# Kernel optimization log

Measured on AMD Instinct MI355X. Metric: run time of the kernel, lower is better.

## Reference

```python
import jax, jax.numpy as jnp
import numpy as np

NUM_HEADS = 16
D_IN = 1024
D_OUT = 64  # = D_IN // NUM_HEADS
N = 2048


def setup_inputs() -> dict:
    key = jax.random.key(0)
    kx, kq, kk, kv, ko = jax.random.split(key, 5)
    x = jax.random.normal(kx, (N, D_IN), dtype=jnp.float32)
    # per-head projection weights, stacked over heads (torch code keeps a
    # Python list of SelfAttention modules; stacking is the vectorized form)
    q_proj = jax.random.normal(kq, (NUM_HEADS, D_IN, D_OUT), dtype=jnp.float32)
    k_proj = jax.random.normal(kk, (NUM_HEADS, D_IN, D_OUT), dtype=jnp.float32)
    v_proj = jax.random.normal(kv, (NUM_HEADS, D_IN, D_OUT), dtype=jnp.float32)
    o_proj = jax.random.normal(ko, (D_IN, D_IN), dtype=jnp.float32)
    return {"x": x, "q_proj": q_proj, "k_proj": k_proj, "v_proj": v_proj, "o_proj": o_proj}


def reference(x, q_proj, k_proj, v_proj, o_proj):
    d_out = q_proj.shape[-1]
    # per-head projections: [H, N, E]
    q = jnp.einsum('nd,hde->hne', x, q_proj)
    k = jnp.einsum('nd,hde->hne', x, k_proj)
    v = jnp.einsum('nd,hde->hne', x, v_proj)
    # full NxN scores per head (matches the naive torch implementation's math)
    scores = jnp.einsum('hne,hme->hnm', q, k) / jnp.sqrt(jnp.float32(d_out))
    attn = jax.nn.softmax(scores, axis=-1)
    ctx = jnp.einsum('hnm,hme->hne', attn, v)
    # concat heads along the feature dim (head 0 first, as in torch.cat)
    h, n, e = ctx.shape
    out = jnp.transpose(ctx, (1, 0, 2)).reshape(n, h * e)
    return out @ o_proj
```

## Files before the change

kernel.cpp:

```cpp
#include <hip/hip_runtime.h>

#define H 16
#define N 2048
#define E 64
#define D 1024

typedef __attribute__((ext_vector_type(8))) short bf16x8;
typedef __attribute__((ext_vector_type(4))) float f32x4;

__device__ __forceinline__ float bf2f(unsigned short u) {
    union { unsigned int i; float f; } v;
    v.i = ((unsigned int)u) << 16;
    return v.f;
}
__device__ __forceinline__ unsigned short f2bf(float f) {
    unsigned int u = __float_as_uint(f);
    return (unsigned short)((u + 0x7fffu + ((u >> 16) & 1u)) >> 16);
}
#define MFMA(a, b, c) __builtin_amdgcn_mfma_f32_16x16x32_bf16(a, b, c, 0, 0, 0)

typedef __attribute__((address_space(3))) unsigned int lds_u32;
typedef const __attribute__((address_space(1))) unsigned int glb_u32;
__device__ __forceinline__ void dma16(const unsigned short* g, unsigned short* l) {
    __builtin_amdgcn_global_load_lds((glb_u32*)g, (lds_u32*)l, 16, 0, 0);
}

__device__ __forceinline__ int sw8(int row, int c)  { return row * 64  + ((c ^ (row & 7)) << 3); }
__device__ __forceinline__ int sw16(int row, int c) { return row * 128 + ((c ^ (row & 7)) << 3); }

__global__ __launch_bounds__(256) void convert_all_kernel(
    const float* __restrict__ x,
    const float* __restrict__ qw, const float* __restrict__ kw,
    const float* __restrict__ vw, const float* __restrict__ ow,
    unsigned short* __restrict__ xh, unsigned short* __restrict__ xl,
    unsigned short* __restrict__ wBh, unsigned short* __restrict__ wBl,
    unsigned short* __restrict__ wvt, unsigned short* __restrict__ woh)
{
    __shared__ float ts[64][65];
    const int b0 = blockIdx.x;
    const int t = threadIdx.x;
    if (b0 < 2048) {
        const int i = (b0 * 256 + t) * 4;
        const float4 v = *(const float4*)&x[i];
        ushort4 hh, ll;
        hh.x = f2bf(v.x); ll.x = f2bf(v.x - bf2f(hh.x));
        hh.y = f2bf(v.y); ll.y = f2bf(v.y - bf2f(hh.y));
        hh.z = f2bf(v.z); ll.z = f2bf(v.z - bf2f(hh.z));
        hh.w = f2bf(v.w); ll.w = f2bf(v.w - bf2f(hh.w));
        *(ushort4*)&xh[i] = hh;
        *(ushort4*)&xl[i] = ll;
        return;
    }
    const int b = b0 - 2048;
    const float* src;
    int rs, dt, orow0;
    bool has_lo;
    unsigned short *dh, *dl;
    if (b < 768) {
        const int which = b >> 8, r = b & 255, h = r >> 4;
        dt = r & 15;
        src = (which == 0 ? qw : which == 1 ? kw : vw) + ((size_t)h * D + dt * 64) * E;
        rs = E;
        if (which == 0)      { dh = wBh; dl = wBl; orow0 = h * 64;        has_lo = true; }
        else if (which == 1) { dh = wBh; dl = wBl; orow0 = 1024 + h * 64; has_lo = true; }
        else                 { dh = wvt; dl = wBl; orow0 = h * 64;        has_lo = false; }
    } else {
        const int r = b - 768, ct = r >> 4;
        dt = r & 15;
        src = ow + (size_t)(dt * 64) * D + ct * 64;
        rs = D;
        orow0 = ct * 64;
        dh = woh; dl = wBl; has_lo = false;
    }
    {
        const int row = t >> 2, cb = (t & 3) * 16;
        #pragma unroll
        for (int j = 0; j < 16; j += 4) {
            const float4 v = *(const float4*)&src[row * rs + cb + j];
            ts[row][cb + j + 0] = v.x;
            ts[row][cb + j + 1] = v.y;
            ts[row][cb + j + 2] = v.z;
            ts[row][cb + j + 3] = v.w;
        }
    }
    __syncthreads();
    {
        const int cl = t >> 2, dp = (t & 3) * 16;
        bf16x8 hv0, hv1, lv0, lv1;
        #pragma unroll
        for (int i = 0; i < 16; ++i) {
            const float f = ts[dp + i][cl];
            const unsigned short hh = f2bf(f);
            const unsigned short lo = f2bf(f - bf2f(hh));
            if (i < 8) { hv0[i] = (short)hh; lv0[i] = (short)lo; }
            else       { hv1[i - 8] = (short)hh; lv1[i - 8] = (short)lo; }
        }
        const size_t o = (size_t)(orow0 + cl) * D + dt * 64 + dp;
        *(bf16x8*)&dh[o] = hv0;
        *(bf16x8*)&dh[o + 8] = hv1;
        if (has_lo) {
            *(bf16x8*)&dl[o] = lv0;
            *(bf16x8*)&dl[o + 8] = lv1;
        }
    }
}

__global__ __launch_bounds__(256, 3) void qkv_kernel(
    const unsigned short* __restrict__ xh, const unsigned short* __restrict__ xl,
    const unsigned short* __restrict__ wBh, const unsigned short* __restrict__ wBl,
    const unsigned short* __restrict__ wvt,
    unsigned short* __restrict__ Qh, unsigned short* __restrict__ Ql,
    unsigned short* __restrict__ Kh, unsigned short* __restrict__ Kl,
    unsigned short* __restrict__ Vt)
{
    __shared__ unsigned short ash[128 * 64], asl[128 * 64];
    __shared__ unsigned short bsh[64 * 64], bsl[64 * 64];
    const int n0 = blockIdx.x * 128;
    const int ct0 = blockIdx.y;
    const int sec = ct0 >> 4;
    const int hh = ct0 & 15;
    const bool isv = (sec == 2);
    const unsigned short* Bh = isv ? wvt : wBh;
    const size_t brow0 = (sec == 1 ? 1024 : 0) + hh * 64;

    const int t = threadIdx.x;
    const int lane = t & 63, wvi = t >> 6, quad = lane >> 4, l15 = lane & 15;

    f32x4 acc[2][4];
    #pragma unroll
    for (int i = 0; i < 2; ++i)
        #pragma unroll
        for (int j = 0; j < 4; ++j) acc[i][j] = (f32x4){0.f, 0.f, 0.f, 0.f};

    for (int k0 = 0; k0 < D; k0 += 64) {
        __syncthreads();
        #pragma unroll
        for (int p = 0; p < 4; ++p) {
            const int row = p * 32 + wvi * 8 + (lane >> 3);
            const int lc = (lane & 7) ^ (row & 7);
            const int lo = p * 2048 + wvi * 512 + lane * 8;
            const size_t ga = (size_t)(n0 + row) * D + k0 + lc * 8;
            dma16(&xh[ga], &ash[lo]);
            if (!isv) dma16(&xl[ga], &asl[lo]);
        }
        #pragma unroll
        for (int p = 0; p < 2; ++p) {
            const int row = p * 32 + wvi * 8 + (lane >> 3);
            const int lc = (lane & 7) ^ (row & 7);
            const int lo = p * 2048 + wvi * 512 + lane * 8;
            const size_t gb = (brow0 + row) * D + k0 + lc * 8;
            dma16(&Bh[gb], &bsh[lo]);
            if (!isv) dma16(&wBl[gb], &bsl[lo]);
        }
        __syncthreads();

        #pragma unroll
        for (int kwi = 0; kwi < 2; ++kwi) {
            const int c = kwi * 4 + quad;
            bf16x8 ah[2], al[2], bh[4], bl[4];
            #pragma unroll
            for (int i = 0; i < 2; ++i) {
                ah[i] = *(const bf16x8*)&ash[sw8(wvi * 32 + i * 16 + l15, c)];
                if (!isv) al[i] = *(const bf16x8*)&asl[sw8(wvi * 32 + i * 16 + l15, c)];
            }
            #pragma unroll
            for (int j = 0; j < 4; ++j) {
                bh[j] = *(const bf16x8*)&bsh[sw8(j * 16 + l15, c)];
                if (!isv) bl[j] = *(const bf16x8*)&bsl[sw8(j * 16 + l15, c)];
            }
            #pragma unroll
            for (int i = 0; i < 2; ++i)
                #pragma unroll
                for (int j = 0; j < 4; ++j) {
                    acc[i][j] = MFMA(ah[i], bh[j], acc[i][j]);
                    if (!isv) {
                        acc[i][j] = MFMA(ah[i], bl[j], acc[i][j]);
                        acc[i][j] = MFMA(al[i], bh[j], acc[i][j]);
                    }
                }
        }
    }

    if (isv) {
        #pragma unroll
        for (int j = 0; j < 4; ++j) {
            const int e = j * 16 + l15;
            #pragma unroll
            for (int i = 0; i < 2; ++i) {
                const int nb = n0 + wvi * 32 + i * 16 + quad * 4;
                ushort4 pk;
                pk.x = f2bf(acc[i][j][0]);
                pk.y = f2bf(acc[i][j][1]);
                pk.z = f2bf(acc[i][j][2]);
                pk.w = f2bf(acc[i][j][3]);
                *(ushort4*)&Vt[((size_t)hh * 64 + e) * N + nb] = pk;
            }
        }
    } else {
        const float scale = (sec == 0) ? 0.125f : 1.0f;
        unsigned short* Oh = (sec == 0) ? Qh : Kh;
        unsigned short* Ol = (sec == 0) ? Ql : Kl;
        #pragma unroll
        for (int j = 0; j < 4; ++j) {
            const int e = j * 16 + l15;
            #pragma unroll
            for (int i = 0; i < 2; ++i)
                #pragma unroll
                for (int r = 0; r < 4; ++r) {
                    const int n = n0 + wvi * 32 + i * 16 + quad * 4 + r;
                    const float val = acc[i][j][r] * scale;
                    const unsigned short hv = f2bf(val);
                    Oh[((size_t)hh * N + n) * E + e] = hv;
                    Ol[((size_t)hh * N + n) * E + e] = f2bf(val - bf2f(hv));
                }
        }
    }
}

__global__ __launch_bounds__(256, 2) void attn_kernel(
    const unsigned short* __restrict__ Qh, const unsigned short* __restrict__ Ql,
    const unsigned short* __restrict__ Kh, const unsigned short* __restrict__ Kl,
    const unsigned short* __restrict__ Vt,
    unsigned short* __restrict__ Ch)
{
    __shared__ unsigned short ksh[128 * 64], ksl[128 * 64];
    __shared__ unsigned short vts[64 * 128];
    __shared__ unsigned short ps[4 * 16 * 136];
    const int r0 = blockIdx.x * 64, h = blockIdx.y;
    const int t = threadIdx.x, lane = t & 63, wvi = t >> 6, quad = lane >> 4, l15 = lane & 15;

    bf16x8 qfh[2], qfl[2];
    {
        const size_t base = ((size_t)h * N + r0 + wvi * 16 + l15) * E;
        #pragma unroll
        for (int kwi = 0; kwi < 2; ++kwi) {
            qfh[kwi] = *(const bf16x8*)&Qh[base + kwi * 32 + quad * 8];
            qfl[kwi] = *(const bf16x8*)&Ql[base + kwi * 32 + quad * 8];
        }
    }

    f32x4 oacc[4];
    #pragma unroll
    for (int ct = 0; ct < 4; ++ct) oacc[ct] = (f32x4){0.f, 0.f, 0.f, 0.f};
    float mrow[4] = {-1e30f, -1e30f, -1e30f, -1e30f};
    float lrow[4] = {0.f, 0.f, 0.f, 0.f};

    for (int m0 = 0; m0 < N; m0 += 128) {
        __syncthreads();
        #pragma unroll
        for (int p = 0; p < 4; ++p) {
            const int row = p * 32 + wvi * 8 + (lane >> 3);
            const int lc = (lane & 7) ^ (row & 7);
            const int lo = p * 2048 + wvi * 512 + lane * 8;
            const size_t gk = ((size_t)h * N + m0 + row) * E + lc * 8;
            dma16(&Kh[gk], &ksh[lo]);
            dma16(&Kl[gk], &ksl[lo]);
        }
        #pragma unroll
        for (int p = 0; p < 4; ++p) {
            const int row = p * 16 + wvi * 4 + (lane >> 4);
            const int lc = (lane & 15) ^ (row & 7);
            const int lo = p * 2048 + wvi * 512 + lane * 8;
            dma16(&Vt[((size_t)h * 64 + row) * N + m0 + lc * 8], &vts[lo]);
        }
        __syncthreads();

        f32x4 s[8];
        #pragma unroll
        for (int ct = 0; ct < 8; ++ct) s[ct] = (f32x4){0.f, 0.f, 0.f, 0.f};
        #pragma unroll
        for (int kwi = 0; kwi < 2; ++kwi) {
            const int c = kwi * 4 + quad;
            #pragma unroll
            for (int ct = 0; ct < 8; ++ct) {
                const bf16x8 bh = *(const bf16x8*)&ksh[sw8(ct * 16 + l15, c)];
                const bf16x8 bl = *(const bf16x8*)&ksl[sw8(ct * 16 + l15, c)];
                s[ct] = MFMA(qfh[kwi], bh, s[ct]);
                s[ct] = MFMA(qfh[kwi], bl, s[ct]);
                s[ct] = MFMA(qfl[kwi], bh, s[ct]);
            }
        }

        #pragma unroll
        for (int r = 0; r < 4; ++r) {
            float mx = s[0][r];
            #pragma unroll
            for (int ct = 1; ct < 8; ++ct) mx = fmaxf(mx, s[ct][r]);
            mx = fmaxf(mx, __shfl_xor(mx, 1));
            mx = fmaxf(mx, __shfl_xor(mx, 2));
            mx = fmaxf(mx, __shfl_xor(mx, 4));
            mx = fmaxf(mx, __shfl_xor(mx, 8));
            const float mn = fmaxf(mrow[r], mx);
            const float alpha = __expf(mrow[r] - mn);
            mrow[r] = mn;
            float sum = 0.f;
            #pragma unroll
            for (int ct = 0; ct < 8; ++ct) {
                const float p = __expf(s[ct][r] - mn);
                s[ct][r] = p;
                sum += p;
            }
            sum += __shfl_xor(sum, 1);
            sum += __shfl_xor(sum, 2);
            sum += __shfl_xor(sum, 4);
            sum += __shfl_xor(sum, 8);
            lrow[r] = lrow[r] * alpha + sum;
            #pragma unroll
            for (int ct = 0; ct < 4; ++ct) oacc[ct][r] *= alpha;
        }

        #pragma unroll
        for (int ct = 0; ct < 8; ++ct)
            #pragma unroll
            for (int r = 0; r < 4; ++r)
                ps[(wvi * 16 + quad * 4 + r) * 136 + ct * 16 + l15] = f2bf(s[ct][r]);

        #pragma unroll
        for (int kwi = 0; kwi < 4; ++kwi) {
            const bf16x8 pa = *(const bf16x8*)&ps[(wvi * 16 + l15) * 136 + kwi * 32 + quad * 8];
            #pragma unroll
            for (int ct = 0; ct < 4; ++ct) {
                const bf16x8 vb = *(const bf16x8*)&vts[sw16(ct * 16 + l15, kwi * 4 + quad)];
                oacc[ct] = MFMA(pa, vb, oacc[ct]);
            }
        }
    }

    #pragma unroll
    for (int r = 0; r < 4; ++r) {
        const float inv = 1.f / lrow[r];
        const int n = r0 + wvi * 16 + quad * 4 + r;
        #pragma unroll
        for (int ct = 0; ct < 4; ++ct)
            Ch[(size_t)n * D + h * 64 + ct * 16 + l15] = f2bf(oacc[ct][r] * inv);
    }
}

__global__ __launch_bounds__(256, 4) void out_proj_kernel(
    const unsigned short* __restrict__ Chh, const unsigned short* __restrict__ Wh,
    float* __restrict__ out)
{
    __shared__ unsigned short ash[64 * 64], bsh[64 * 64];
    const int n0 = blockIdx.x * 64, c0 = blockIdx.y * 64;
    const int t = threadIdx.x, lane = t & 63, wvi = t >> 6, quad = lane >> 4, l15 = lane & 15;

    f32x4 acc[4];
    #pragma unroll
    for (int j = 0; j < 4; ++j) acc[j] = (f32x4){0.f, 0.f, 0.f, 0.f};

    for (int k0 = 0; k0 < D; k0 += 64) {
        __syncthreads();
        #pragma unroll
        for (int p = 0; p < 2; ++p) {
            const int row = p * 32 + wvi * 8 + (lane >> 3);
            const int lc = (lane & 7) ^ (row & 7);
            const int lo = p * 2048 + wvi * 512 + lane * 8;
            dma16(&Chh[(size_t)(n0 + row) * D + k0 + lc * 8], &ash[lo]);
            dma16(&Wh[(size_t)(c0 + row) * D + k0 + lc * 8], &bsh[lo]);
        }
        __syncthreads();

        #pragma unroll
        for (int kwi = 0; kwi < 2; ++kwi) {
            const int c = kwi * 4 + quad;
            const bf16x8 ah = *(const bf16x8*)&ash[sw8(wvi * 16 + l15, c)];
            #pragma unroll
            for (int j = 0; j < 4; ++j) {
                const bf16x8 bh = *(const bf16x8*)&bsh[sw8(j * 16 + l15, c)];
                acc[j] = MFMA(ah, bh, acc[j]);
            }
        }
    }

    #pragma unroll
    for (int r = 0; r < 4; ++r) {
        const int n = n0 + wvi * 16 + quad * 4 + r;
        #pragma unroll
        for (int j = 0; j < 4; ++j)
            out[(size_t)n * D + c0 + j * 16 + l15] = acc[j][r];
    }
}

extern "C" void kernel_launch(void* const* d_in, const int* in_sizes, int n_in,
                              void* d_out, int out_size, void* d_ws, size_t ws_size,
                              hipStream_t stream) {
    const float* x  = (const float*)d_in[0];
    const float* qw = (const float*)d_in[1];
    const float* kw = (const float*)d_in[2];
    const float* vw = (const float*)d_in[3];
    const float* ow = (const float*)d_in[4];
    float* out = (float*)d_out;

    unsigned short* ws = (unsigned short*)d_ws;
    const size_t M1 = 1024 * 1024;
    unsigned short* wBh = ws;
    unsigned short* wBl = ws + 2 * M1;
    unsigned short* wvt = ws + 4 * M1;
    unsigned short* woh = ws + 5 * M1;
    unsigned short* xh  = ws + 6 * M1;
    unsigned short* xl  = ws + 8 * M1;
    unsigned short* Qh  = ws + 10 * M1;
    unsigned short* Ql  = ws + 12 * M1;
    unsigned short* Kh  = ws + 14 * M1;
    unsigned short* Kl  = ws + 16 * M1;
    unsigned short* Vt  = ws + 18 * M1;
    unsigned short* Ch  = xh;

    convert_all_kernel<<<3072, 256, 0, stream>>>(x, qw, kw, vw, ow,
                                                 xh, xl, wBh, wBl, wvt, woh);
    qkv_kernel<<<dim3(16, 48), 256, 0, stream>>>(xh, xl, wBh, wBl, wvt,
                                                 Qh, Ql, Kh, Kl, Vt);
    attn_kernel<<<dim3(32, 16), 256, 0, stream>>>(Qh, Ql, Kh, Kl, Vt, Ch);
    out_proj_kernel<<<dim3(32, 16), 256, 0, stream>>>(Ch, woh, out);
}
```

Before: 181.1 us.

## Double-buffer K/V tiles in attention with fp16 PV and exp2 softmax

Restructures the attention loop to use 64-key tiles with a two-stage LDS double buffer, so the DMA for the next K/V tile is issued before computing the current one and one barrier per iteration is removed. V and P switch from bf16 to fp16 (packed RTZ conversion) for the PV MFMA, which gives more mantissa precision. The log2(e) factor is folded into the Q scale so softmax can use exp2f. Smaller tiles cut LDS use and register pressure but double the loop trip count, and overlap correctness depends on the barrier placement before each buffer is reused.

```diff
diff --git a/kernel.cpp b/kernel.cpp
--- a/kernel.cpp
+++ b/kernel.cpp
@@ -6,6 +6,8 @@
 #define D 1024
 
 typedef __attribute__((ext_vector_type(8))) short bf16x8;
+typedef __attribute__((ext_vector_type(8))) _Float16 f16x8;
+typedef __attribute__((ext_vector_type(2))) __fp16 fp16v2;
 typedef __attribute__((ext_vector_type(4))) float f32x4;
 
 __device__ __forceinline__ float bf2f(unsigned short u) {
@@ -17,7 +19,8 @@
     unsigned int u = __float_as_uint(f);
     return (unsigned short)((u + 0x7fffu + ((u >> 16) & 1u)) >> 16);
 }
-#define MFMA(a, b, c) __builtin_amdgcn_mfma_f32_16x16x32_bf16(a, b, c, 0, 0, 0)
+#define MFMA(a, b, c)  __builtin_amdgcn_mfma_f32_16x16x32_bf16(a, b, c, 0, 0, 0)
+#define MFMAH(a, b, c) __builtin_amdgcn_mfma_f32_16x16x32_f16(a, b, c, 0, 0, 0)
 
 typedef __attribute__((address_space(3))) unsigned int lds_u32;
 typedef const __attribute__((address_space(1))) unsigned int glb_u32;
@@ -26,7 +29,6 @@
 }
 
 __device__ __forceinline__ int sw8(int row, int c)  { return row * 64  + ((c ^ (row & 7)) << 3); }
-__device__ __forceinline__ int sw16(int row, int c) { return row * 128 + ((c ^ (row & 7)) << 3); }
 
 __global__ __launch_bounds__(256) void convert_all_kernel(
     const float* __restrict__ x,
@@ -188,16 +190,15 @@
             #pragma unroll
             for (int i = 0; i < 2; ++i) {
                 const int nb = n0 + wvi * 32 + i * 16 + quad * 4;
-                ushort4 pk;
-                pk.x = f2bf(acc[i][j][0]);
-                pk.y = f2bf(acc[i][j][1]);
-                pk.z = f2bf(acc[i][j][2]);
-                pk.w = f2bf(acc[i][j][3]);
-                *(ushort4*)&Vt[((size_t)hh * 64 + e) * N + nb] = pk;
+                union { fp16v2 h; unsigned int u; } c01, c23;
+                c01.h = __builtin_amdgcn_cvt_pkrtz(acc[i][j][0], acc[i][j][1]);
+                c23.h = __builtin_amdgcn_cvt_pkrtz(acc[i][j][2], acc[i][j][3]);
+                uint2 pk = {c01.u, c23.u};
+                *(uint2*)&Vt[((size_t)hh * 64 + e) * N + nb] = pk;
             }
         }
     } else {
-        const float scale = (sec == 0) ? 0.125f : 1.0f;
+        const float scale = (sec == 0) ? 0.125f * 1.44269504f : 1.0f;
         unsigned short* Oh = (sec == 0) ? Qh : Kh;
         unsigned short* Ol = (sec == 0) ? Ql : Kl;
         #pragma unroll
@@ -223,11 +224,13 @@
     const unsigned short* __restrict__ Vt,
     unsigned short* __restrict__ Ch)
 {
-    __shared__ unsigned short ksh[128 * 64], ksl[128 * 64];
-    __shared__ unsigned short vts[64 * 128];
-    __shared__ unsigned short ps[4 * 16 * 136];
+    __shared__ unsigned short kb[2][3][64 * 64];
+    __shared__ unsigned short ps[4 * 16 * 72];
     const int r0 = blockIdx.x * 64, h = blockIdx.y;
     const int t = threadIdx.x, lane = t & 63, wvi = t >> 6, quad = lane >> 4, l15 = lane & 15;
+
+    const int srow0 = wvi * 8 + (lane >> 3);
+    const int slo0  = wvi * 512 + lane * 8;
 
     bf16x8 qfh[2], qfl[2];
     {
@@ -245,36 +248,44 @@
     float mrow[4] = {-1e30f, -1e30f, -1e30f, -1e30f};
     float lrow[4] = {0.f, 0.f, 0.f, 0.f};
 
-    for (int m0 = 0; m0 < N; m0 += 128) {
+    #pragma unroll
+    for (int p = 0; p < 2; ++p) {
+        const int row = p * 32 + srow0;
+        const int lc = (lane & 7) ^ (row & 7);
+        const int lo = p * 2048 + slo0;
+        const size_t gk = ((size_t)h * N + row) * E + lc * 8;
+        dma16(&Kh[gk], &kb[0][0][lo]);
+        dma16(&Kl[gk], &kb[0][1][lo]);
+        dma16(&Vt[((size_t)h * 64 + row) * N + lc * 8], &kb[0][2][lo]);
+    }
+
+    for (int mt = 0; mt < N / 64; ++mt) {
+        const int b = mt & 1;
         __syncthreads();
-        #pragma unroll
-        for (int p = 0; p < 4; ++p) {
-            const int row = p * 32 + wvi * 8 + (lane >> 3);
-            const int lc = (lane & 7) ^ (row & 7);
-            const int lo = p * 2048 + wvi * 512 + lane * 8;
-            const size_t gk = ((size_t)h * N + m0 + row) * E + lc * 8;
-            dma16(&Kh[gk], &ksh[lo]);
-            dma16(&Kl[gk], &ksl[lo]);
-        }
-        #pragma unroll
-        for (int p = 0; p < 4; ++p) {
-            const int row = p * 16 + wvi * 4 + (lane >> 4);
-            const int lc = (lane & 15) ^ (row & 7);
-            const int lo = p * 2048 + wvi * 512 + lane * 8;
-            dma16(&Vt[((size_t)h * 64 + row) * N + m0 + lc * 8], &vts[lo]);
-        }
-        __syncthreads();
-
-        f32x4 s[8];
-        #pragma unroll
-        for (int ct = 0; ct < 8; ++ct) s[ct] = (f32x4){0.f, 0.f, 0.f, 0.f};
+        if (mt + 1 < N / 64) {
+            const int m1 = (mt + 1) * 64;
+            #pragma unroll
+            for (int p = 0; p < 2; ++p) {
+                const int row = p * 32 + srow0;
+                const int lc = (lane & 7) ^ (row & 7);
+                const int lo = p * 2048 + slo0;
+                const size_t gk = ((size_t)h * N + m1 + row) * E + lc * 8;
+                dma16(&Kh[gk], &kb[1 - b][0][lo]);
+                dma16(&Kl[gk], &kb[1 - b][1][lo]);
+                dma16(&Vt[((size_t)h * 64 + row) * N + m1 + lc * 8], &kb[1 - b][2][lo]);
+            }
+        }
+
+        f32x4 s[4];
+        #pragma unroll
+        for (int ct = 0; ct < 4; ++ct) s[ct] = (f32x4){0.f, 0.f, 0.f, 0.f};
         #pragma unroll
         for (int kwi = 0; kwi < 2; ++kwi) {
             const int c = kwi * 4 + quad;
             #pragma unroll
-            for (int ct = 0; ct < 8; ++ct) {
-                const bf16x8 bh = *(const bf16x8*)&ksh[sw8(ct * 16 + l15, c)];
-                const bf16x8 bl = *(const bf16x8*)&ksl[sw8(ct * 16 + l15, c)];
+            for (int ct = 0; ct < 4; ++ct) {
+                const bf16x8 bh = *(const bf16x8*)&kb[b][0][sw8(ct * 16 + l15, c)];
+                const bf16x8 bl = *(const bf16x8*)&kb[b][1][sw8(ct * 16 + l15, c)];
                 s[ct] = MFMA(qfh[kwi], bh, s[ct]);
                 s[ct] = MFMA(qfh[kwi], bl, s[ct]);
                 s[ct] = MFMA(qfl[kwi], bh, s[ct]);
@@ -283,20 +294,18 @@
 
         #pragma unroll
         for (int r = 0; r < 4; ++r) {
-            float mx = s[0][r];
-            #pragma unroll
-            for (int ct = 1; ct < 8; ++ct) mx = fmaxf(mx, s[ct][r]);
+            float mx = fmaxf(fmaxf(s[0][r], s[1][r]), fmaxf(s[2][r], s[3][r]));
             mx = fmaxf(mx, __shfl_xor(mx, 1));
             mx = fmaxf(mx, __shfl_xor(mx, 2));
             mx = fmaxf(mx, __shfl_xor(mx, 4));
             mx = fmaxf(mx, __shfl_xor(mx, 8));
             const float mn = fmaxf(mrow[r], mx);
-            const float alpha = __expf(mrow[r] - mn);
+            const float alpha = exp2f(mrow[r] - mn);
             mrow[r] = mn;
             float sum = 0.f;
             #pragma unroll
-            for (int ct = 0; ct < 8; ++ct) {
-                const float p = __expf(s[ct][r] - mn);
+            for (int ct = 0; ct < 4; ++ct) {
+                const float p = exp2f(s[ct][r] - mn);
                 s[ct][r] = p;
                 sum += p;
             }
@@ -310,18 +319,21 @@
         }
 
         #pragma unroll
-        for (int ct = 0; ct < 8; ++ct)
-            #pragma unroll
-            for (int r = 0; r < 4; ++r)
-                ps[(wvi * 16 + quad * 4 + r) * 136 + ct * 16 + l15] = f2bf(s[ct][r]);
-
-        #pragma unroll
-        for (int kwi = 0; kwi < 4; ++kwi) {
-            const bf16x8 pa = *(const bf16x8*)&ps[(wvi * 16 + l15) * 136 + kwi * 32 + quad * 8];
+        for (int ct = 0; ct < 4; ++ct)
+            #pragma unroll
+            for (int r = 0; r < 4; ++r) {
+                union { _Float16 h; unsigned short u; } cv;
+                cv.h = (_Float16)s[ct][r];
+                ps[(wvi * 16 + quad * 4 + r) * 72 + ct * 16 + l15] = cv.u;
+            }
+
+        #pragma unroll
+        for (int kwi = 0; kwi < 2; ++kwi) {
+            const f16x8 pa = *(const f16x8*)&ps[(wvi * 16 + l15) * 72 + kwi * 32 + quad * 8];
             #pragma unroll
             for (int ct = 0; ct < 4; ++ct) {
-                const bf16x8 vb = *(const bf16x8*)&vts[sw16(ct * 16 + l15, kwi * 4 + quad)];
-                oacc[ct] = MFMA(pa, vb, oacc[ct]);
+                const f16x8 vb = *(const f16x8*)&kb[b][2][sw8(ct * 16 + l15, kwi * 4 + quad)];
+                oacc[ct] = MFMAH(pa, vb, oacc[ct]);
             }
         }
     }
```

Result: slower. 198.0 us (+9.3%).
